# Optimization experiments

Hardware: AMD Instinct MI355X
Metric: run time of the kernel (lower is better)

The kernel has to match this reference:

```python
import jax, jax.numpy as jnp
import numpy as np

N = 1536
NUM_SPECIES = 8
HIDDEN = 64
NUM_CENTERS = 32
CUTOFF = 5.0
RBF_GAMMA = 4.0  # 1 / width^2, width = 0.5
CENTERS = jnp.linspace(0.0, CUTOFF, NUM_CENTERS, dtype=jnp.float32)
PAIR_IN = NUM_CENTERS + HIDDEN                       # 96
LOCAL_IN = NUM_CENTERS * NUM_SPECIES + HIDDEN // 2 + 1  # 289


def cutoff_fn(d):
    x = jnp.clip(d / CUTOFF, 0.0, 1.0)
    return jnp.where(d < CUTOFF, 0.5 * (jnp.cos(jnp.pi * x) + 1.0), jnp.zeros_like(d))


def rbf_fn(d):
    return jnp.exp(-RBF_GAMMA * (d[..., None] - CENTERS) ** 2)


def mlp3(x, W1, b1, W2, b2, W3, b3):
    h = jax.nn.silu(x @ W1 + b1)
    h = jax.nn.silu(h @ W2 + b2)
    return h @ W3 + b3


def setup_inputs() -> dict:
    key = jax.random.key(0)
    ks = jax.random.split(key, 20)
    s = 0.1
    d = {
        "species": jax.random.randint(ks[0], (N,), 0, NUM_SPECIES, dtype=jnp.int32),
        "positions": jax.random.normal(ks[1], (N, 3), jnp.float32) * 4.0,
        "total_charge": jax.random.normal(ks[2], (1,), jnp.float32),
        "embed": jax.random.normal(ks[3], (NUM_SPECIES, HIDDEN // 2), jnp.float32) * s,
        "W1": jax.random.normal(ks[4], (PAIR_IN, HIDDEN), jnp.float32) * s,
        "b1": jnp.zeros((HIDDEN,), jnp.float32),
        "W2": jax.random.normal(ks[5], (HIDDEN, HIDDEN), jnp.float32) * s,
        "b2": jnp.zeros((HIDDEN,), jnp.float32),
        "W3": jax.random.normal(ks[6], (HIDDEN, 1), jnp.float32) * s,
        "b3": jnp.zeros((1,), jnp.float32),
        "atom_bias": jax.random.normal(ks[7], (NUM_SPECIES, 1), jnp.float32) * s,
        "cW1": jax.random.normal(ks[8], (LOCAL_IN, HIDDEN), jnp.float32) * s,
        "cb1": jnp.zeros((HIDDEN,), jnp.float32),
        "cW2": jax.random.normal(ks[9], (HIDDEN, HIDDEN), jnp.float32) * s,
        "cb2": jnp.zeros((HIDDEN,), jnp.float32),
        "cW3": jax.random.normal(ks[10], (HIDDEN, 1), jnp.float32) * s,
        "cb3": jnp.zeros((1,), jnp.float32),
        "charge_scale": jnp.float32(1.0),
        "coulomb_scale": jnp.float32(1.0),
        "softening_raw": jnp.float32(-3.0),
    }
    return d


def reference(species, positions, total_charge, embed, W1, b1, W2, b2, W3, b3,
              atom_bias, cW1, cb1, cW2, cb2, cW3, cb3,
              charge_scale, coulomb_scale, softening_raw):
    n = positions.shape[0]
    diff = positions[:, None, :] - positions[None, :, :]          # [n,n,3]
    dist = jnp.sqrt((diff ** 2).sum(-1) + 1e-12)                  # [n,n]
    iu0, iu1 = jnp.triu_indices(n, k=1)
    rij = dist[iu0, iu1]                                          # [P]
    cut = cutoff_fn(rij)
    ei = embed[species[iu0]]
    ej = embed[species[iu1]]
    pair_feat = jnp.concatenate([rbf_fn(rij), ei + ej, ei * ej], axis=-1)  # [P,96]
    pair_energy = mlp3(pair_feat, W1, b1, W2, b2, W3, b3)[:, 0]
    energy = jnp.sum(pair_energy * cut) + atom_bias[species].sum()

    # --- latent charges ---
    cut_mat = cutoff_fn(dist) * (1.0 - jnp.eye(n, dtype=dist.dtype))
    basis = rbf_fn(dist) * cut_mat[..., None]                     # [n,n,K]
    one_hot = jax.nn.one_hot(species, NUM_SPECIES, dtype=dist.dtype)
    local = jnp.einsum('ijk,jc->ick', basis, one_hot).reshape(n, -1)  # [n, S*K]
    x = jnp.concatenate([local, embed[species],
                         jnp.broadcast_to(total_charge, (n, 1))], axis=-1)
    raw = mlp3(x, cW1, cb1, cW2, cb2, cW3, cb3)[:, 0] * charge_scale
    charges = raw - raw.mean() + total_charge[0] / n
    soft = jax.nn.softplus(softening_raw) + 0.001
    energy_lr = coulomb_scale * jnp.sum(charges[iu0] * charges[iu1]
                                        / jnp.sqrt(rij ** 2 + soft ** 2))
    energy = energy + energy_lr
    return (energy, charges)
```

## Files before the change

### kernel.cpp

```cpp
#include <hip/hip_runtime.h>
#include <math.h>

#define NATOMS 1536
#define NSPEC 8
#define HID 64
#define NCEN 32
#define CUTOFF_R 5.0f
#define PI_F 3.14159265358979323846f
#define NBR_CAP 1024
#define PREP_BLOCKS 65
#define PAIR_B 768
#define TAIL_GRID 1024

typedef __attribute__((ext_vector_type(8))) short short8;
typedef __attribute__((ext_vector_type(4))) float float4v;

__device__ __forceinline__ float silu_f(float x) {
    return x / (1.f + __expf(-x));
}
__device__ __forceinline__ short f2bf(float x) {
    unsigned u = __float_as_uint(x);
    u += 0x7fffu + ((u >> 16) & 1u);
    return (short)(u >> 16);
}
__device__ __forceinline__ float cut_f(float d) {
    return 0.5f * (__cosf((PI_F / CUTOFF_R) * d) + 1.f);
}

__global__ __launch_bounds__(256) void k_local(
    const int* __restrict__ species, const float* __restrict__ pos,
    const float* __restrict__ tq, const float* __restrict__ embed,
    const float* __restrict__ cW1, const float* __restrict__ cb1,
    const float* __restrict__ cW2, const float* __restrict__ cb2,
    const float* __restrict__ cW3, const float* __restrict__ cb3,
    const float* __restrict__ charge_scale,
    const float* __restrict__ W1, const float* __restrict__ b1,
    const float* __restrict__ W2,
    float* __restrict__ ctab, short* __restrict__ bw1, short* __restrict__ bw2,
    float* __restrict__ raw, double* __restrict__ rsum,
    unsigned int* __restrict__ pcount, uint2* __restrict__ pdlist)
{
    __shared__ float2 dc_l[NBR_CAP];
    __shared__ unsigned short spj_l[NBR_CAP];
    __shared__ unsigned short pj_l[NBR_CAP];
    __shared__ float s_part[8 * 256];
    __shared__ float s_x[292];
    __shared__ float s_h[64];
    __shared__ unsigned n_cnt, p_cnt, s_base;

    const int t = threadIdx.x;

    if (blockIdx.x >= NATOMS) {
        const int b = blockIdx.x - NATOMS;
        if (b < 64) {
            if (t < 64) {
                const int c = b;
                const int si2 = c >> 3, sj2 = c & 7;
                const int o = t;
                float acc = b1[o];
                #pragma unroll 4
                for (int k = 0; k < 32; k++) {
                    const float a = embed[si2 * 32 + k];
                    const float bb = embed[sj2 * 32 + k];
                    acc += (a + bb) * W1[(32 + k) * HID + o];
                    acc += (a * bb) * W1[(64 + k) * HID + o];
                }
                ctab[c * HID + o] = acc;
            }
        } else {
            for (int e = t; e < 2048; e += 256) {
                const int tile = e >> 9, L = (e >> 3) & 63, j = e & 7;
                const int k = (L >> 4) * 8 + j;
                const int n = tile * 16 + (L & 15);
                bw1[e] = f2bf(W1[k * HID + n]);
            }
            for (int e = t; e < 4096; e += 256) {
                const int ct = e >> 9, L = (e >> 3) & 63, j = e & 7;
                const int c = ct >> 2, tile = ct & 3;
                const int k = c * 32 + (L >> 4) * 8 + j;
                const int n = tile * 16 + (L & 15);
                bw2[e] = f2bf(W2[k * HID + n]);
            }
        }
        return;
    }

    const int i = blockIdx.x;
    const int lane = t & 63;
    if (t == 0) { n_cnt = 0u; p_cnt = 0u; }
    __syncthreads();

    const float xi = pos[3*i+0], yi = pos[3*i+1], zi = pos[3*i+2];
    const int si = species[i];

    #pragma unroll
    for (int j0 = 0; j0 < NATOMS; j0 += 256) {
        const int j = j0 + t;
        const float dx = xi - pos[3*j+0];
        const float dy = yi - pos[3*j+1];
        const float dz = zi - pos[3*j+2];
        const float d = sqrtf(dx*dx + dy*dy + dz*dz + 1e-12f);
        const bool within = (d < CUTOFF_R) && (j != i);
        const unsigned long long m = __ballot((int)within);
        if (within) {
            const unsigned prefix = (unsigned)__popcll(m & ((1ull << lane) - 1ull));
            unsigned base = 0;
            if (prefix == 0) base = atomicAdd(&n_cnt, (unsigned)__popcll(m));
            base = (unsigned)__builtin_amdgcn_readfirstlane((int)base);
            const unsigned ofs = base + prefix;
            if (ofs < NBR_CAP) {
                dc_l[ofs] = make_float2(d, cut_f(d));
                spj_l[ofs] = (unsigned short)((species[j] << 11) | j);
            }
        }
    }
    __syncthreads();
    const unsigned cnt = (n_cnt < NBR_CAP) ? n_cnt : NBR_CAP;

    for (unsigned n0 = 0; n0 < cnt; n0 += 256) {
        const unsigned n = n0 + (unsigned)t;
        bool app = false;
        if (n < cnt) app = ((int)(spj_l[n] & 2047u) > i);
        const unsigned long long m = __ballot((int)app);
        if (app) {
            const unsigned prefix = (unsigned)__popcll(m & ((1ull << lane) - 1ull));
            unsigned base = 0;
            if (prefix == 0) base = atomicAdd(&p_cnt, (unsigned)__popcll(m));
            base = (unsigned)__builtin_amdgcn_readfirstlane((int)base);
            pj_l[base + prefix] = (unsigned short)n;
        }
    }
    __syncthreads();
    if (t == 0) s_base = atomicAdd(pcount, p_cnt);
    __syncthreads();
    {
        const unsigned pc = p_cnt, base = s_base;
        for (unsigned idx = (unsigned)t; idx < pc; idx += 256) {
            const unsigned n = pj_l[idx];
            const unsigned w = spj_l[n];
            const unsigned jj = w & 2047u, spj = w >> 11;
            uint2 pd;
            pd.x = (((unsigned)si * 8u + spj) << 22) | ((unsigned)i << 11) | jj;
            pd.y = __float_as_uint(dc_l[n].x);
            pdlist[base + idx] = pd;
        }
    }

    {
        const int k = t & 31, gg = t >> 5;
        const float ck = (float)k * (CUTOFF_R / 31.f);
        float f0=0.f,f1=0.f,f2=0.f,f3=0.f,f4=0.f,f5=0.f,f6=0.f,f7=0.f;
        #pragma unroll 2
        for (unsigned n = (unsigned)gg; n < cnt; n += 8) {
            const float2 dc = dc_l[n];
            const float diff = dc.x - ck;
            const float v = __expf(-4.f * diff * diff) * dc.y;
            const int sp = (int)(spj_l[n] >> 11);
            f0 += (sp == 0) ? v : 0.f;
            f1 += (sp == 1) ? v : 0.f;
            f2 += (sp == 2) ? v : 0.f;
            f3 += (sp == 3) ? v : 0.f;
            f4 += (sp == 4) ? v : 0.f;
            f5 += (sp == 5) ? v : 0.f;
            f6 += (sp == 6) ? v : 0.f;
            f7 += (sp == 7) ? v : 0.f;
        }
        float* sp_g = &s_part[gg * 256 + k];
        sp_g[0*32] = f0; sp_g[1*32] = f1; sp_g[2*32] = f2; sp_g[3*32] = f3;
        sp_g[4*32] = f4; sp_g[5*32] = f5; sp_g[6*32] = f6; sp_g[7*32] = f7;
    }
    __syncthreads();
    {
        float acc = 0.f;
        #pragma unroll
        for (int g2 = 0; g2 < 8; g2++) acc += s_part[g2 * 256 + t];
        s_x[t] = acc;
        if (t < 32) s_x[256 + t] = embed[si * 32 + t];
        if (t == 0) s_x[288] = tq[0];
    }
    __syncthreads();

    {
        const int g3 = t >> 6, o = t & 63;
        const int k0 = g3 * 72;
        const int k1 = (g3 == 3) ? 289 : (k0 + 72);
        float acc = 0.f;
        #pragma unroll 8
        for (int k = k0; k < k1; k++) acc += s_x[k] * cW1[k * 64 + o];
        s_part[g3 * 64 + o] = acc;
    }
    __syncthreads();
    if (t < 64) {
        const float a = cb1[t] + s_part[t] + s_part[64 + t]
                      + s_part[128 + t] + s_part[192 + t];
        s_h[t] = silu_f(a);
    }
    __syncthreads();
    {
        const int g3 = t >> 6, o = t & 63;
        float acc = 0.f;
        #pragma unroll
        for (int kk = 0; kk < 16; kk++) {
            const int k = g3 * 16 + kk;
            acc += s_h[k] * cW2[k * 64 + o];
        }
        s_part[g3 * 64 + o] = acc;
    }
    __syncthreads();
    if (t < 64) {
        const float a = cb2[t] + s_part[t] + s_part[64 + t]
                      + s_part[128 + t] + s_part[192 + t];
        float v = silu_f(a) * cW3[t];
        #pragma unroll
        for (int off = 32; off > 0; off >>= 1) v += __shfl_down(v, off);
        if (t == 0) {
            const float rawv = (v + cb3[0]) * charge_scale[0];
            raw[i] = rawv;
            atomicAdd(rsum, (double)rawv);
        }
    }
}

__global__ __launch_bounds__(256, 4) void k_tail(
    const int* __restrict__ species, const float* __restrict__ pos,
    const float* __restrict__ raw, const float* __restrict__ tq,
    const float* __restrict__ softening, const float* __restrict__ atom_bias,
    const float* __restrict__ coulomb_scale,
    const float* __restrict__ b2, const float* __restrict__ W3,
    const float* __restrict__ b3, const float* __restrict__ ctab,
    const short* __restrict__ bw1, const short* __restrict__ bw2,
    const unsigned int* __restrict__ pcount, const uint2* __restrict__ pdlist,
    const double* __restrict__ rsum,
    double* __restrict__ epp, double* __restrict__ elp,
    double* __restrict__ bias_part, unsigned int* __restrict__ done,
    float* __restrict__ out_energy, float* __restrict__ charges)
{
    __shared__ float s_tp[4][16 * 66];
    __shared__ float s_red[256];
    __shared__ double s_redd[256];
    __shared__ unsigned s_ticket;
    const int t = threadIdx.x;
    const int lane = t & 63;

    if (blockIdx.x < PAIR_B) {
        const int wid = t >> 6;
        const int col = lane & 15;
        const int quad = lane >> 4;
        const short8* __restrict__ bw1v = (const short8*)bw1;
        const short8* __restrict__ bw2v = (const short8*)bw2;
        short8 w1f[4], w2f[8];
        #pragma unroll
        for (int t4 = 0; t4 < 4; t4++) w1f[t4] = bw1v[t4 * 64 + lane];
        #pragma unroll
        for (int q8 = 0; q8 < 8; q8++) w2f[q8] = bw2v[q8 * 64 + lane];
        float b2l[4], w3l[4];
        #pragma unroll
        for (int t4 = 0; t4 < 4; t4++) { b2l[t4] = b2[t4*16+col]; w3l[t4] = W3[t4*16+col]; }
        const float b3v = b3[0];
        const unsigned cnt = *pcount;
        float* tb = &s_tp[wid][0];

        float esum = 0.f;
        const unsigned wstep = PAIR_B * 4u;
        for (unsigned w = blockIdx.x * 4u + (unsigned)wid; w * 16u < cnt; w += wstep) {
            unsigned p_idx = w * 16u + (unsigned)col;
            const bool valid = p_idx < cnt;
            if (!valid) p_idx = cnt - 1;
            const uint2 pd = pdlist[p_idx];
            const int combo = (int)(pd.x >> 22);
            const float d = __uint_as_float(pd.y);
            const float cut = valid ? cut_f(d) : 0.f;
            if (lane < 16) esum += b3v * cut;

            short8 a1f;
            #pragma unroll
            for (int jj = 0; jj < 8; jj++) {
                const float ck = (float)(quad * 8 + jj) * (CUTOFF_R / 31.f);
                const float diff = d - ck;
                a1f[jj] = f2bf(__expf(-4.f * diff * diff));
            }

            int cmb[4]; float cutr[4];
            #pragma unroll
            for (int r = 0; r < 4; r++) {
                const int p = quad * 4 + r;
                cmb[r]  = __shfl(combo, p);
                cutr[r] = __shfl(cut, p);
            }

            float4v acc[4];
            #pragma unroll
            for (int t4 = 0; t4 < 4; t4++) {
                #pragma unroll
                for (int r = 0; r < 4; r++)
                    acc[t4][r] = ctab[cmb[r] * HID + t4 * 16 + col];
            }
            #pragma unroll
            for (int t4 = 0; t4 < 4; t4++)
                acc[t4] = __builtin_amdgcn_mfma_f32_16x16x32_bf16(a1f, w1f[t4], acc[t4], 0, 0, 0);

            #pragma unroll
            for (int t4 = 0; t4 < 4; t4++) {
                #pragma unroll
                for (int r = 0; r < 4; r++)
                    tb[(quad * 4 + r) * 66 + t4 * 16 + col] = silu_f(acc[t4][r]);
            }
            short8 a2f[2];
            #pragma unroll
            for (int c = 0; c < 2; c++) {
                #pragma unroll
                for (int jj = 0; jj < 8; jj++)
                    a2f[c][jj] = f2bf(tb[col * 66 + c * 32 + quad * 8 + jj]);
            }

            float4v acc2[4];
            #pragma unroll
            for (int t4 = 0; t4 < 4; t4++) {
                acc2[t4][0] = b2l[t4]; acc2[t4][1] = b2l[t4];
                acc2[t4][2] = b2l[t4]; acc2[t4][3] = b2l[t4];
            }
            #pragma unroll
            for (int c = 0; c < 2; c++) {
                #pragma unroll
                for (int t4 = 0; t4 < 4; t4++)
                    acc2[t4] = __builtin_amdgcn_mfma_f32_16x16x32_bf16(a2f[c], w2f[c*4+t4], acc2[t4], 0, 0, 0);
            }

            #pragma unroll
            for (int r = 0; r < 4; r++) {
                float part = 0.f;
                #pragma unroll
                for (int t4 = 0; t4 < 4; t4++) part += silu_f(acc2[t4][r]) * w3l[t4];
                esum += part * cutr[r];
            }
        }

        s_red[t] = esum;
        __syncthreads();
        for (int s = 128; s > 0; s >>= 1) { if (t < s) s_red[t] += s_red[t + s]; __syncthreads(); }
        if (t == 0)
            atomicExch((unsigned long long*)&epp[blockIdx.x],
                       (unsigned long long)__double_as_longlong((double)s_red[0]));
    } else {
        const int b = blockIdx.x - PAIR_B;
        const float mean = (float)(rsum[0] / (double)NATOMS);
        const float add = tq[0] / (float)NATOMS;

        if (b == 0) {
            float acc = 0.f;
            for (int idx = t; idx < NATOMS; idx += 256) acc += atom_bias[species[idx]];
            s_red[t] = acc;
            __syncthreads();
            for (int s = 128; s > 0; s >>= 1) { if (t < s) s_red[t] += s_red[t + s]; __syncthreads(); }
            if (t == 0)
                atomicExch((unsigned long long*)bias_part,
                           (unsigned long long)__double_as_longlong((double)s_red[0]));
            __syncthreads();
        }

        const int gid = b * 256 + t;
        if (gid < NATOMS) charges[gid] = raw[gid] - mean + add;

        const float sr = softening[0];
        const float sp = ((sr > 20.f) ? sr : log1pf(__expf(sr))) + 0.001f;
        const float sp2 = sp * sp;
        float acc = 0.f;
        for (int i = b; i < NATOMS; i += 256) {
            const float xi = pos[3*i+0], yi = pos[3*i+1], zi = pos[3*i+2];
            const float qi = raw[i] - mean + add;
            for (int j = i + 1 + t; j < NATOMS; j += 256) {
                const float dx = xi - pos[3*j+0];
                const float dy = yi - pos[3*j+1];
                const float dz = zi - pos[3*j+2];
                const float d2 = dx*dx + dy*dy + dz*dz + 1e-12f;
                const float qj = raw[j] - mean + add;
                acc += qi * qj * rsqrtf(d2 + sp2);
            }
        }
        s_red[t] = acc;
        __syncthreads();
        for (int s = 128; s > 0; s >>= 1) { if (t < s) s_red[t] += s_red[t + s]; __syncthreads(); }
        if (t == 0)
            atomicExch((unsigned long long*)&elp[b],
                       (unsigned long long)__double_as_longlong((double)s_red[0]));
    }

    if (t == 0) {
        __threadfence();
        s_ticket = atomicAdd(done, 1u);
    }
    __syncthreads();
    if (s_ticket == (unsigned)TAIL_GRID - 1u) {
        __threadfence();
        const double cs = (double)coulomb_scale[0];
        double acc = 0.0;
        for (int idx = t; idx < PAIR_B; idx += 256)
            acc += __longlong_as_double(
                (long long)atomicAdd((unsigned long long*)&epp[idx], 0ull));
        if (t < 256) {
            acc += cs * __longlong_as_double(
                (long long)atomicAdd((unsigned long long*)&elp[t], 0ull));
        }
        s_redd[t] = acc;
        __syncthreads();
        for (int s = 128; s > 0; s >>= 1) { if (t < s) s_redd[t] += s_redd[t + s]; __syncthreads(); }
        if (t == 0) {
            const double bd = __longlong_as_double(
                (long long)atomicAdd((unsigned long long*)bias_part, 0ull));
            out_energy[0] = (float)(s_redd[0] + bd);
        }
    }
}

extern "C" void kernel_launch(void* const* d_in, const int* in_sizes, int n_in,
                              void* d_out, int out_size, void* d_ws, size_t ws_size,
                              hipStream_t stream) {
    const int*   species       = (const int*)d_in[0];
    const float* pos           = (const float*)d_in[1];
    const float* tq            = (const float*)d_in[2];
    const float* embed         = (const float*)d_in[3];
    const float* W1            = (const float*)d_in[4];
    const float* b1            = (const float*)d_in[5];
    const float* W2            = (const float*)d_in[6];
    const float* b2            = (const float*)d_in[7];
    const float* W3            = (const float*)d_in[8];
    const float* b3            = (const float*)d_in[9];
    const float* atom_bias     = (const float*)d_in[10];
    const float* cW1           = (const float*)d_in[11];
    const float* cb1           = (const float*)d_in[12];
    const float* cW2           = (const float*)d_in[13];
    const float* cb2           = (const float*)d_in[14];
    const float* cW3           = (const float*)d_in[15];
    const float* cb3           = (const float*)d_in[16];
    const float* charge_scale  = (const float*)d_in[17];
    const float* coulomb_scale = (const float*)d_in[18];
    const float* softening     = (const float*)d_in[19];

    char* ws = (char*)d_ws;
    double*   rsum      = (double*)(ws + 0);
    double*   bias_part = (double*)(ws + 8);
    unsigned* pcount    = (unsigned*)(ws + 16);
    unsigned* done      = (unsigned*)(ws + 20);
    float*    raw       = (float*)(ws + 64);
    float*    ctab      = (float*)(ws + 8192);
    short*    bw1       = (short*)(ws + 24576);
    short*    bw2       = (short*)(ws + 28672);
    double*   epp       = (double*)(ws + 36864);
    double*   elp       = (double*)(ws + 43008);
    uint2*    pdlist    = (uint2*)(ws + 49152);

    float* out     = (float*)d_out;
    float* charges = out + 1;

    hipMemsetAsync(d_ws, 0, 24, stream);

    k_local<<<NATOMS + PREP_BLOCKS, 256, 0, stream>>>(
        species, pos, tq, embed,
        cW1, cb1, cW2, cb2, cW3, cb3, charge_scale,
        W1, b1, W2, ctab, bw1, bw2,
        raw, rsum, pcount, pdlist);
    k_tail<<<TAIL_GRID, 256, 0, stream>>>(
        species, pos, raw, tq, softening, atom_bias, coulomb_scale,
        b2, W3, b3, ctab, bw1, bw2, pcount, pdlist, rsum,
        epp, elp, bias_part, done, out, charges);
}
```

Measured before the change: 166.4 us.

## Split charge MLP into separate kernel batching 8 atoms per block

Moves the per-atom charge MLP out of the neighbor-feature kernel into a new kernel that processes 8 atoms per block. Each loaded cW1/cW2 weight is reused across 8 atoms instead of one, and the rsum atomics drop by a factor of 8. In exchange, the 289-float features per atom are written to global workspace and read back, and an extra kernel launch is added.

```diff
diff --git a/kernel.cpp b/kernel.cpp
--- a/kernel.cpp
+++ b/kernel.cpp
@@ -9,6 +9,8 @@
 #define PI_F 3.14159265358979323846f
 #define NBR_CAP 1024
 #define PREP_BLOCKS 65
+#define AP 8
+#define CHG_BLOCKS (NATOMS / AP)
 #define PAIR_B 768
 #define TAIL_GRID 1024
 
@@ -27,25 +29,19 @@
     return 0.5f * (__cosf((PI_F / CUTOFF_R) * d) + 1.f);
 }
 
-__global__ __launch_bounds__(256) void k_local(
+__global__ __launch_bounds__(256) void k_nbr(
     const int* __restrict__ species, const float* __restrict__ pos,
     const float* __restrict__ tq, const float* __restrict__ embed,
-    const float* __restrict__ cW1, const float* __restrict__ cb1,
-    const float* __restrict__ cW2, const float* __restrict__ cb2,
-    const float* __restrict__ cW3, const float* __restrict__ cb3,
-    const float* __restrict__ charge_scale,
     const float* __restrict__ W1, const float* __restrict__ b1,
     const float* __restrict__ W2,
     float* __restrict__ ctab, short* __restrict__ bw1, short* __restrict__ bw2,
-    float* __restrict__ raw, double* __restrict__ rsum,
+    float* __restrict__ xfeat,
     unsigned int* __restrict__ pcount, uint2* __restrict__ pdlist)
 {
     __shared__ float2 dc_l[NBR_CAP];
     __shared__ unsigned short spj_l[NBR_CAP];
     __shared__ unsigned short pj_l[NBR_CAP];
     __shared__ float s_part[8 * 256];
-    __shared__ float s_x[292];
-    __shared__ float s_h[64];
     __shared__ unsigned n_cnt, p_cnt, s_base;
 
     const int t = threadIdx.x;
@@ -174,50 +170,92 @@
         float acc = 0.f;
         #pragma unroll
         for (int g2 = 0; g2 < 8; g2++) acc += s_part[g2 * 256 + t];
-        s_x[t] = acc;
-        if (t < 32) s_x[256 + t] = embed[si * 32 + t];
-        if (t == 0) s_x[288] = tq[0];
-    }
+        xfeat[i * 292 + t] = acc;
+        if (t < 32) xfeat[i * 292 + 256 + t] = embed[si * 32 + t];
+        if (t == 0) xfeat[i * 292 + 288] = tq[0];
+    }
+}
+
+__global__ __launch_bounds__(256) void k_charge(
+    const float* __restrict__ xfeat,
+    const float* __restrict__ cW1, const float* __restrict__ cb1,
+    const float* __restrict__ cW2, const float* __restrict__ cb2,
+    const float* __restrict__ cW3, const float* __restrict__ cb3,
+    const float* __restrict__ charge_scale,
+    float* __restrict__ raw, double* __restrict__ rsum)
+{
+    __shared__ float s_xx[AP][292];
+    __shared__ float s_p[4][AP][64];
+    __shared__ float s_h[AP][64];
+    __shared__ float s_rawl[AP];
+
+    const int t = threadIdx.x;
+    const int a0 = blockIdx.x * AP;
+    const int g3 = t >> 6, o = t & 63;
+
+    #pragma unroll
+    for (int a = 0; a < AP; a++)
+        for (int e = t; e < 289; e += 256)
+            s_xx[a][e] = xfeat[(a0 + a) * 292 + e];
     __syncthreads();
 
     {
-        const int g3 = t >> 6, o = t & 63;
         const int k0 = g3 * 72;
         const int k1 = (g3 == 3) ? 289 : (k0 + 72);
-        float acc = 0.f;
-        #pragma unroll 8
-        for (int k = k0; k < k1; k++) acc += s_x[k] * cW1[k * 64 + o];
-        s_part[g3 * 64 + o] = acc;
-    }
-    __syncthreads();
-    if (t < 64) {
-        const float a = cb1[t] + s_part[t] + s_part[64 + t]
-                      + s_part[128 + t] + s_part[192 + t];
-        s_h[t] = silu_f(a);
-    }
-    __syncthreads();
+        float acc[AP] = {0.f,0.f,0.f,0.f,0.f,0.f,0.f,0.f};
+        #pragma unroll 4
+        for (int k = k0; k < k1; k++) {
+            const float w = cW1[k * 64 + o];
+            #pragma unroll
+            for (int a = 0; a < AP; a++) acc[a] += s_xx[a][k] * w;
+        }
+        #pragma unroll
+        for (int a = 0; a < AP; a++) s_p[g3][a][o] = acc[a];
+    }
+    __syncthreads();
+    #pragma unroll
+    for (int aa = 0; aa < 2; aa++) {
+        const int a = g3 * 2 + aa;
+        const float v = cb1[o] + s_p[0][a][o] + s_p[1][a][o]
+                      + s_p[2][a][o] + s_p[3][a][o];
+        s_h[a][o] = silu_f(v);
+    }
+    __syncthreads();
+
     {
-        const int g3 = t >> 6, o = t & 63;
-        float acc = 0.f;
+        float acc[AP] = {0.f,0.f,0.f,0.f,0.f,0.f,0.f,0.f};
         #pragma unroll
         for (int kk = 0; kk < 16; kk++) {
             const int k = g3 * 16 + kk;
-            acc += s_h[k] * cW2[k * 64 + o];
-        }
-        s_part[g3 * 64 + o] = acc;
-    }
-    __syncthreads();
-    if (t < 64) {
-        const float a = cb2[t] + s_part[t] + s_part[64 + t]
-                      + s_part[128 + t] + s_part[192 + t];
-        float v = silu_f(a) * cW3[t];
-        #pragma unroll
-        for (int off = 32; off > 0; off >>= 1) v += __shfl_down(v, off);
-        if (t == 0) {
-            const float rawv = (v + cb3[0]) * charge_scale[0];
-            raw[i] = rawv;
-            atomicAdd(rsum, (double)rawv);
-        }
+            const float w = cW2[k * 64 + o];
+            #pragma unroll
+            for (int a = 0; a < AP; a++) acc[a] += s_h[a][k] * w;
+        }
+        #pragma unroll
+        for (int a = 0; a < AP; a++) s_p[g3][a][o] = acc[a];
+    }
+    __syncthreads();
+
+    #pragma unroll
+    for (int aa = 0; aa < 2; aa++) {
+        const int a = g3 * 2 + aa;
+        const float v = cb2[o] + s_p[0][a][o] + s_p[1][a][o]
+                      + s_p[2][a][o] + s_p[3][a][o];
+        float r = silu_f(v) * cW3[o];
+        #pragma unroll
+        for (int off = 32; off > 0; off >>= 1) r += __shfl_down(r, off);
+        if (o == 0) {
+            const float rawv = (r + cb3[0]) * charge_scale[0];
+            raw[a0 + a] = rawv;
+            s_rawl[a] = rawv;
+        }
+    }
+    __syncthreads();
+    if (t == 0) {
+        double srp = 0.0;
+        #pragma unroll
+        for (int a = 0; a < AP; a++) srp += (double)s_rawl[a];
+        atomicAdd(rsum, srp);
     }
 }
 
@@ -447,18 +485,19 @@
     short*    bw2       = (short*)(ws + 28672);
     double*   epp       = (double*)(ws + 36864);
     double*   elp       = (double*)(ws + 43008);
-    uint2*    pdlist    = (uint2*)(ws + 49152);
+    float*    xfeat     = (float*)(ws + 49152);
+    uint2*    pdlist    = (uint2*)(ws + 1843200);
 
     float* out     = (float*)d_out;
     float* charges = out + 1;
 
     hipMemsetAsync(d_ws, 0, 24, stream);
 
-    k_local<<<NATOMS + PREP_BLOCKS, 256, 0, stream>>>(
-        species, pos, tq, embed,
-        cW1, cb1, cW2, cb2, cW3, cb3, charge_scale,
-        W1, b1, W2, ctab, bw1, bw2,
-        raw, rsum, pcount, pdlist);
+    k_nbr<<<NATOMS + PREP_BLOCKS, 256, 0, stream>>>(
+        species, pos, tq, embed, W1, b1, W2,
+        ctab, bw1, bw2, xfeat, pcount, pdlist);
+    k_charge<<<CHG_BLOCKS, 256, 0, stream>>>(
+        xfeat, cW1, cb1, cW2, cb2, cW3, cb3, charge_scale, raw, rsum);
     k_tail<<<TAIL_GRID, 256, 0, stream>>>(
         species, pos, raw, tq, softening, atom_bias, coulomb_scale,
         b2, W3, b3, ctab, bw1, bw2, pcount, pdlist, rsum,
```

Measured after the change: 180.8 us. 8.7% more time.
